# Performance work log

Hardware: AMD Instinct MI355X
Metric: run time of the kernel (lower is better)

## Reference

```python
import jax, jax.numpy as jnp
import numpy as np

GUMBEL_BETA = 0.0036  # gumbel_beta init kwarg
N1, N2, BOX_DIM = 160, 1024, 256


def _center_sigmoid_offsets(data):
    # CenterSigmoidBoxTensor: softplus with beta=10, then sigmoid
    sp = jax.nn.softplus(10.0 * data[..., 1, :]) / 10.0
    zmin = jax.nn.sigmoid(data[..., 0, :] - sp)
    zmax = jax.nn.sigmoid(data[..., 0, :] + sp)
    return zmin, zmax


def setup_inputs() -> dict:
    key = jax.random.key(0)
    k1, k2 = jax.random.split(key)
    box1s = jax.random.normal(k1, (N1, 2, BOX_DIM), dtype=jnp.float32)
    box2s = jax.random.normal(k2, (N2, 2, BOX_DIM), dtype=jnp.float32)
    return {"box1s": box1s, "box2s": box2s}


def reference(box1s, box2s):
    gb = GUMBEL_BETA
    z1, Z1 = _center_sigmoid_offsets(box1s)  # [N1, D]
    z2, Z2 = _center_sigmoid_offsets(box2s)  # [N2, D]

    # Pairwise: i over box2s (outer), j over box1s (inner) -> [N2, N1, D]
    a, b = z2[:, None, :], z1[None, :, :]
    # gb * logsumexp([a/gb, b/gb], 0) == max(a,b) + gb*log1p(exp(-|a-b|/gb))
    lse_min = jnp.maximum(a, b) + gb * jnp.log1p(jnp.exp(-jnp.abs(a - b) / gb))
    inter_min = jnp.maximum(lse_min, jnp.maximum(a, b))

    A, B = Z2[:, None, :], Z1[None, :, :]
    # -gb * logsumexp([-A/gb, -B/gb], 0) == min(A,B) - gb*log1p(exp(-|A-B|/gb))
    lse_max = jnp.minimum(A, B) - gb * jnp.log1p(jnp.exp(-jnp.abs(A - B) / gb))
    inter_max = jnp.minimum(lse_max, jnp.minimum(A, B))

    n2, n1, d = inter_min.shape
    return inter_min.reshape(n2 * n1, d), inter_max.reshape(n2 * n1, d)
```

## Files before the change

kernel.cpp:

```cpp
#include <hip/hip_runtime.h>

#define BN1 160
#define BN2 1024
#define BD  256

#define GB_LN2 0.0024953256f
#define K2     400.74862f

typedef float f32x4 __attribute__((ext_vector_type(4)));

#define EXP2F(x) __builtin_amdgcn_exp2f(x)
#define LOG2F(x) __builtin_amdgcn_logf(x)

__device__ float g_z1min[BN1 * BD];
__device__ float g_z1max[BN1 * BD];
__device__ float g_z2min[BN2 * BD];
__device__ float g_z2max[BN2 * BD];

__device__ __forceinline__ float softplus10(float x) {
    float y = 10.0f * x;
    float t = __expf(-fabsf(y));
    return (fmaxf(y, 0.0f) + __logf(1.0f + t)) * 0.1f;
}

__device__ __forceinline__ float sigmoidf(float x) {
    return 1.0f / (1.0f + __expf(-x));
}

__global__ __launch_bounds__(256) void precompute_kernel(
        const float* __restrict__ box1s, const float* __restrict__ box2s) {
    int idx = blockIdx.x * 256 + threadIdx.x;
    if (idx < BN2 * BD) {
        int n = idx >> 8;
        int d = idx & (BD - 1);
        float c  = box2s[n * 2 * BD + d];
        float sp = softplus10(box2s[n * 2 * BD + BD + d]);
        g_z2min[idx] = sigmoidf(c - sp);
        g_z2max[idx] = sigmoidf(c + sp);
    } else {
        int j = idx - BN2 * BD;
        if (j < BN1 * BD) {
            int n = j >> 8;
            int d = j & (BD - 1);
            float c  = box1s[n * 2 * BD + d];
            float sp = softplus10(box1s[n * 2 * BD + BD + d]);
            g_z1min[j] = sigmoidf(c - sp);
            g_z1max[j] = sigmoidf(c + sp);
        }
    }
}

union F4 {
    f32x4 v;
    float f[4];
};

__device__ __forceinline__ float gumbel_min(float x, float y) {
    float m = fmaxf(x, y);
    float c = GB_LN2 * LOG2F(1.0f + EXP2F(-fabsf(x - y) * K2));
    return fmaxf(m + c, m);
}

__device__ __forceinline__ float gumbel_max(float x, float y) {
    float m = fminf(x, y);
    float c = GB_LN2 * LOG2F(1.0f + EXP2F(-fabsf(x - y) * K2));
    return fminf(m - c, m);
}

__global__ __launch_bounds__(256) void pairs_kernel(float* __restrict__ out) {
    const int t   = threadIdx.x;
    const int bid = blockIdx.x;
    const int i2  = bid / 20;
    const int i1  = (bid - i2 * 20) * 8 + ((t >> 6) << 1);
    const int d0  = (t & 63) << 2;

    F4 a, A, b0, B0, b1, B1;
    a.v  = *(const f32x4*)(g_z2min + i2 * BD + d0);
    A.v  = *(const f32x4*)(g_z2max + i2 * BD + d0);
    b0.v = *(const f32x4*)(g_z1min + i1 * BD + d0);
    B0.v = *(const f32x4*)(g_z1max + i1 * BD + d0);
    b1.v = *(const f32x4*)(g_z1min + (i1 + 1) * BD + d0);
    B1.v = *(const f32x4*)(g_z1max + (i1 + 1) * BD + d0);

    F4 o00, o01, o10, o11;
#pragma unroll
    for (int j = 0; j < 4; ++j) {
        const float av = a.f[j], Av = A.f[j];
        o00.f[j] = gumbel_min(av, b0.f[j]);
        o01.f[j] = gumbel_max(Av, B0.f[j]);
        o10.f[j] = gumbel_min(av, b1.f[j]);
        o11.f[j] = gumbel_max(Av, B1.f[j]);
    }

    const size_t half = (size_t)BN2 * BN1 * BD;
    const size_t base = (size_t)(i2 * BN1 + i1) * BD + d0;
    __builtin_nontemporal_store(o00.v, (f32x4*)(out + base));
    __builtin_nontemporal_store(o10.v, (f32x4*)(out + base + BD));
    __builtin_nontemporal_store(o01.v, (f32x4*)(out + half + base));
    __builtin_nontemporal_store(o11.v, (f32x4*)(out + half + base + BD));
}

extern "C" void kernel_launch(void* const* d_in, const int* in_sizes, int n_in,
                              void* d_out, int out_size, void* d_ws, size_t ws_size,
                              hipStream_t stream) {
    const float* box1s = (const float*)d_in[0];
    const float* box2s = (const float*)d_in[1];
    float* out = (float*)d_out;

    precompute_kernel<<<1184, 256, 0, stream>>>(box1s, box2s);

    pairs_kernel<<<BN2 * (BN1 / 8), 256, 0, stream>>>(out);
}
```

Baseline: 332.4 us.

## Process eight box1 rows per wave with prefetching and XCD-aware block remap

Each wave now handles eight consecutive (i2,i1) output rows instead of two, so each z2 row is loaded once and reused across eight box1 rows, with the next box1 row prefetched while the current one is computed. Block IDs are permuted so consecutive logical blocks are spread across the eight XCDs. Stores switch from nontemporal to regular. The grid shrinks from 20480 to 5120 blocks, so per-thread work rises and there is less parallelism to hide memory latency.

```diff
diff --git a/kernel.cpp b/kernel.cpp
--- a/kernel.cpp
+++ b/kernel.cpp
@@ -68,36 +68,43 @@
 }
 
 __global__ __launch_bounds__(256) void pairs_kernel(float* __restrict__ out) {
-    const int t   = threadIdx.x;
-    const int bid = blockIdx.x;
-    const int i2  = bid / 20;
-    const int i1  = (bid - i2 * 20) * 8 + ((t >> 6) << 1);
-    const int d0  = (t & 63) << 2;
+    const int t    = threadIdx.x;
+    const int wave = t >> 6;
+    const int lane = t & 63;
+    const int bid  = (blockIdx.x & 7) * 640 + (blockIdx.x >> 3);
+    const int r0   = (bid * 4 + wave) * 8;
+    const int i2   = r0 / BN1;
+    const int i1_0 = r0 - i2 * BN1;
+    const int d0   = lane << 2;
 
-    F4 a, A, b0, B0, b1, B1;
-    a.v  = *(const f32x4*)(g_z2min + i2 * BD + d0);
-    A.v  = *(const f32x4*)(g_z2max + i2 * BD + d0);
-    b0.v = *(const f32x4*)(g_z1min + i1 * BD + d0);
-    B0.v = *(const f32x4*)(g_z1max + i1 * BD + d0);
-    b1.v = *(const f32x4*)(g_z1min + (i1 + 1) * BD + d0);
-    B1.v = *(const f32x4*)(g_z1max + (i1 + 1) * BD + d0);
-
-    F4 o00, o01, o10, o11;
-#pragma unroll
-    for (int j = 0; j < 4; ++j) {
-        const float av = a.f[j], Av = A.f[j];
-        o00.f[j] = gumbel_min(av, b0.f[j]);
-        o01.f[j] = gumbel_max(Av, B0.f[j]);
-        o10.f[j] = gumbel_min(av, b1.f[j]);
-        o11.f[j] = gumbel_max(Av, B1.f[j]);
-    }
+    F4 a, A;
+    a.v = *(const f32x4*)(g_z2min + i2 * BD + d0);
+    A.v = *(const f32x4*)(g_z2max + i2 * BD + d0);
 
     const size_t half = (size_t)BN2 * BN1 * BD;
-    const size_t base = (size_t)(i2 * BN1 + i1) * BD + d0;
-    __builtin_nontemporal_store(o00.v, (f32x4*)(out + base));
-    __builtin_nontemporal_store(o10.v, (f32x4*)(out + base + BD));
-    __builtin_nontemporal_store(o01.v, (f32x4*)(out + half + base));
-    __builtin_nontemporal_store(o11.v, (f32x4*)(out + half + base + BD));
+    size_t base = (size_t)r0 * BD + d0;
+
+    F4 b, B, bn, Bn;
+    bn.v = *(const f32x4*)(g_z1min + i1_0 * BD + d0);
+    Bn.v = *(const f32x4*)(g_z1max + i1_0 * BD + d0);
+
+#pragma unroll
+    for (int i = 0; i < 8; ++i) {
+        b = bn; B = Bn;
+        if (i < 7) {
+            bn.v = *(const f32x4*)(g_z1min + (i1_0 + i + 1) * BD + d0);
+            Bn.v = *(const f32x4*)(g_z1max + (i1_0 + i + 1) * BD + d0);
+        }
+        F4 o0, o1;
+#pragma unroll
+        for (int j = 0; j < 4; ++j) {
+            o0.f[j] = gumbel_min(a.f[j], b.f[j]);
+            o1.f[j] = gumbel_max(A.f[j], B.f[j]);
+        }
+        *(f32x4*)(out + base)        = o0.v;
+        *(f32x4*)(out + half + base) = o1.v;
+        base += BD;
+    }
 }
 
 extern "C" void kernel_launch(void* const* d_in, const int* in_sizes, int n_in,
@@ -109,5 +116,5 @@
 
     precompute_kernel<<<1184, 256, 0, stream>>>(box1s, box2s);
 
-    pairs_kernel<<<BN2 * (BN1 / 8), 256, 0, stream>>>(out);
+    pairs_kernel<<<5120, 256, 0, stream>>>(out);
 }
```

New measurement: 328.3 us. About the same (-1.2%).
